# Optimization experiments

Measured on AMD Instinct MI355X. Metric: run time of the kernel, lower is better.

## Reference

```python
import jax, jax.numpy as jnp
from jax import lax
import numpy as np

B, L = 4096, 512
H = 32       # GRU hidden_dim
HH = 32      # hazard_hidden_dim
EPS = 1e-8


def setup_inputs() -> dict:
    key = jax.random.key(0)
    ks = jax.random.split(key, 12)
    s_ih = 1.0 / np.sqrt(H)
    s_l1 = 1.0 / np.sqrt(1 + H)
    s_l2 = 1.0 / np.sqrt(HH)
    return {
        "deltas": jax.random.uniform(ks[0], (B, L), dtype=jnp.float32),
        "mask": jnp.ones((B, L), dtype=jnp.float32),
        # GRUCell params (torch layout: [3H, in], [3H, H], biases [3H]; gates r,z,n)
        "w_ih": jax.random.uniform(ks[1], (3 * H, 1), jnp.float32, -s_ih, s_ih),
        "w_hh": jax.random.uniform(ks[2], (3 * H, H), jnp.float32, -s_ih, s_ih),
        "b_ih": jax.random.uniform(ks[3], (3 * H,), jnp.float32, -s_ih, s_ih),
        "b_hh": jax.random.uniform(ks[4], (3 * H,), jnp.float32, -s_ih, s_ih),
        # hazard MLP: Linear(1+H -> HH), tanh, Linear(HH -> 1)
        "w1": jax.random.uniform(ks[5], (HH, 1 + H), jnp.float32, -s_l1, s_l1),
        "b1": jax.random.uniform(ks[6], (HH,), jnp.float32, -s_l1, s_l1),
        "w2": jax.random.uniform(ks[7], (HH,), jnp.float32, -s_l2, s_l2),
        "b2": jax.random.uniform(ks[8], (1,), jnp.float32, -s_l2, s_l2),
    }


def reference(deltas, mask, w_ih, w_hh, b_ih, b_hh, w1, b1, w2, b2):
    dtype = deltas.dtype
    h0 = jnp.zeros((deltas.shape[0], H), dtype)  # init_hidden_scale == 0 -> zeros
    w1_tau = w1[:, 0]      # [HH] weight on tau column
    w1_h = w1[:, 1:]       # [HH, H]

    def step(carry, xs):
        h, tot = carry
        tau, m = xs                                   # each [B]
        # cumulative hazard phi(tau, h) = softplus(MLP([tau; h]))
        pre = tau[:, None] * w1_tau + h @ w1_h.T + b1  # [B, HH]
        a = jnp.tanh(pre)
        raw = a @ w2 + b2[0]                           # [B]
        phi = jax.nn.softplus(raw)
        # analytic d phi / d tau  (== torch.autograd.grad of phi.sum() wrt tau)
        dphi = jax.nn.sigmoid(raw) * (((1.0 - a * a) * w1_tau) @ w2)
        lam = jax.nn.softplus(dphi) + EPS
        tot = tot + jnp.sum((jnp.log(lam) - phi) * m)
        # GRUCell update with input tau (scalar input_size=1)
        gi = tau[:, None] * w_ih[:, 0] + b_ih          # [B, 3H]
        gh = h @ w_hh.T + b_hh                         # [B, 3H]
        i_r, i_z, i_n = jnp.split(gi, 3, axis=1)
        h_r, h_z, h_n = jnp.split(gh, 3, axis=1)
        r = jax.nn.sigmoid(i_r + h_r)
        z = jax.nn.sigmoid(i_z + h_z)
        n = jnp.tanh(i_n + r * h_n)
        new_h = (1.0 - z) * n + z * h
        me = m[:, None]
        h = me * new_h + (1.0 - me) * h
        return (h, tot), None

    (_, tot), _ = lax.scan(step, (h0, jnp.asarray(0.0, dtype)), (deltas.T, mask.T))
    return tot / (jnp.sum(mask) + EPS)
```

## Files before the change

kernel.cpp:

```cpp
#include <hip/hip_runtime.h>
#include <math.h>


constexpr int Bn = 4096;
constexpr int Ln = 512;
constexpr float EPSf = 1e-8f;
constexpr float LOG2E  = 1.44269504088896f;
constexpr float S2     = 2.0f * LOG2E;

typedef _Float16 f16x8 __attribute__((ext_vector_type(8)));
typedef float    f32x4 __attribute__((ext_vector_type(4)));

__device__ __forceinline__ float aexp2(float x) {
    float r;
    asm volatile("v_exp_f32 %0, %1" : "=v"(r) : "v"(x));
    return r;
}
__device__ __forceinline__ float arcp(float x) {
    float r;
    asm volatile("v_rcp_f32 %0, %1" : "=v"(r) : "v"(x));
    return r;
}

__device__ __forceinline__ float softplusf_(float x) {
    return fmaxf(x, 0.0f) + __logf(1.0f + __expf(-fabsf(x)));
}
__device__ __forceinline__ float sigmoidf_(float x) {
    return __fdividef(1.0f, 1.0f + __expf(-x));
}

union PK2 { _Float16 f[2]; unsigned u; };

__global__ __launch_bounds__(128, 1)
void tpp_main(const float* __restrict__ deltas,
              const float* __restrict__ mask,
              const float* __restrict__ w_ih,
              const float* __restrict__ w_hh,
              const float* __restrict__ b_ih,
              const float* __restrict__ b_hh,
              const float* __restrict__ w1,
              const float* __restrict__ b1,
              const float* __restrict__ w2,
              const float* __restrict__ b2,
              float* __restrict__ partials)
{
    const int tid = threadIdx.x;
    const int w   = tid >> 6;
    const int l   = tid & 63;
    const int c   = l & 15;
    const int g   = l >> 4;
    const int b0  = blockIdx.x * 16;

    __shared__ float2   tm[16][514];
    __shared__ unsigned ibuf[16 * 520];
    __shared__ f16x8    bfbuf[2][16][16][5];

    for (int q = tid; q < 16 * 128; q += 128) {
        const int cc = q >> 7;
        const int t4 = (q & 127) << 2;
        const float4 dv = *(const float4*)(deltas + (size_t)(b0 + cc) * Ln + t4);
        const float4 mv = *(const float4*)(mask   + (size_t)(b0 + cc) * Ln + t4);
        tm[cc][t4 + 0] = make_float2(dv.x, mv.x);
        tm[cc][t4 + 1] = make_float2(dv.y, mv.y);
        tm[cc][t4 + 2] = make_float2(dv.z, mv.z);
        tm[cc][t4 + 3] = make_float2(dv.w, mv.w);
    }

    f16x8 Af[6];
    float wrAn[8], wrBn[8], wzAn[8], wzBn[8];
    float wnA[8], wnB[8];
    f32x4 Cn0 = {}, Cn1 = {};
    float hreg[8];
    f16x8 Afp[2];
    float wpA[8], wpB[8];
    float w2v[8], civ[8], civs = 0.0f, b2v = 0.0f;

    const int ub = 8 * (c >> 2) + (c & 3);
    const int j0 = 8 * g;
    if (w == 0) {
#pragma unroll
        for (int T = 0; T < 6; ++T) {
            const int G = T >> 1, p = T & 1;
            const int up = ub + 4 * p;
            const float sc = (G < 2) ? -LOG2E : S2;
            const float* src =
                (G == 0) ? (w_hh + (size_t)up * 32 + j0) :
                (G == 1) ? (w_hh + (size_t)(32 + up) * 32 + j0) :
                           (w_hh + (size_t)(64 + up) * 32 + j0);
#pragma unroll
            for (int e = 0; e < 8; ++e) Af[T][e] = (_Float16)(src[e] * sc);
        }
#pragma unroll
        for (int e = 0; e < 8; ++e) {
            const int u = 8 * g + e;
            wrAn[e] = -w_ih[u] * LOG2E;
            wrBn[e] = -(b_ih[u] + b_hh[u]) * LOG2E;
            wzAn[e] = -w_ih[32 + u] * LOG2E;
            wzBn[e] = -(b_ih[32 + u] + b_hh[32 + u]) * LOG2E;
            wnA[e]  = w_ih[64 + u] * S2;
            wnB[e]  = b_ih[64 + u] * S2;
            hreg[e] = 0.0f;
        }
#pragma unroll
        for (int d = 0; d < 4; ++d) {
            Cn0[d] = b_hh[64 + 8 * g + d] * S2;
            Cn1[d] = b_hh[64 + 8 * g + 4 + d] * S2;
        }
    } else {
#pragma unroll
        for (int p = 0; p < 2; ++p) {
            const int up = ub + 4 * p;
            const float* src = w1 + (size_t)up * 33 + 1 + j0;
#pragma unroll
            for (int e = 0; e < 8; ++e) Afp[p][e] = (_Float16)(src[e] * S2);
        }
#pragma unroll
        for (int e = 0; e < 8; ++e) {
            const int u = 8 * g + e;
            wpA[e] = w1[(size_t)u * 33] * S2;
            wpB[e] = b1[u] * S2;
            w2v[e] = w2[u];
            civ[e] = w1[(size_t)u * 33] * w2v[e];
            civs  += civ[e];
        }
        b2v = b2[0];
    }

    __syncthreads();

    constexpr int NC = Ln / 16;

    f32x4 Cr0, Cr1, Cz0, Cz1;
    float nbase[8];
    float mcur = 0.0f;
    if (w == 0) {
        const float2 t0v = tm[c][0];
        mcur = t0v.y;
#pragma unroll
        for (int d = 0; d < 4; ++d) {
            Cr0[d] = fmaf(t0v.x, wrAn[d],     wrBn[d]);
            Cr1[d] = fmaf(t0v.x, wrAn[4 + d], wrBn[4 + d]);
            Cz0[d] = fmaf(t0v.x, wzAn[d],     wzBn[d]);
            Cz1[d] = fmaf(t0v.x, wzAn[4 + d], wzBn[4 + d]);
        }
#pragma unroll
        for (int e = 0; e < 8; ++e) nbase[e] = fmaf(t0v.x, wnA[e], wnB[e]);
    }

    for (int chunk = 0; chunk <= NC; ++chunk) {
        if (w == 0 && chunk < NC) {
            const int tbase = chunk * 16;
            for (int s = 0; s < 16; ++s) {
                const int t = tbase + s;

                f16x8 bf;
#pragma unroll
                for (int e2 = 0; e2 < 4; ++e2) {
                    const auto pp = __builtin_amdgcn_cvt_pkrtz(hreg[2 * e2], hreg[2 * e2 + 1]);
                    bf[2 * e2]     = (_Float16)pp[0];
                    bf[2 * e2 + 1] = (_Float16)pp[1];
                }
                bfbuf[chunk & 1][s][c][g] = bf;

                f32x4 ar0 = __builtin_amdgcn_mfma_f32_16x16x32_f16(Af[0], bf, Cr0, 0, 0, 0);
                f32x4 ar1 = __builtin_amdgcn_mfma_f32_16x16x32_f16(Af[1], bf, Cr1, 0, 0, 0);
                f32x4 az0 = __builtin_amdgcn_mfma_f32_16x16x32_f16(Af[2], bf, Cz0, 0, 0, 0);
                f32x4 az1 = __builtin_amdgcn_mfma_f32_16x16x32_f16(Af[3], bf, Cz1, 0, 0, 0);
                f32x4 an0 = __builtin_amdgcn_mfma_f32_16x16x32_f16(Af[4], bf, Cn0, 0, 0, 0);
                f32x4 an1 = __builtin_amdgcn_mfma_f32_16x16x32_f16(Af[5], bf, Cn1, 0, 0, 0);

                const float2 tmn = tm[c][(t + 1 < Ln) ? (t + 1) : t];
                f32x4 Nr0, Nr1, Nz0, Nz1;
                float nbn[8];
#pragma unroll
                for (int d = 0; d < 4; ++d) {
                    Nr0[d] = fmaf(tmn.x, wrAn[d],     wrBn[d]);
                    Nr1[d] = fmaf(tmn.x, wrAn[4 + d], wrBn[4 + d]);
                    Nz0[d] = fmaf(tmn.x, wzAn[d],     wzBn[d]);
                    Nz1[d] = fmaf(tmn.x, wzAn[4 + d], wzBn[4 + d]);
                }
#pragma unroll
                for (int e = 0; e < 8; ++e) nbn[e] = fmaf(tmn.x, wnA[e], wnB[e]);

                float er[8], ez[8];
#pragma unroll
                for (int d = 0; d < 4; ++d) er[d]     = aexp2(ar0[d]);
#pragma unroll
                for (int d = 0; d < 4; ++d) er[4 + d] = aexp2(ar1[d]);
#pragma unroll
                for (int d = 0; d < 4; ++d) ez[d]     = aexp2(az0[d]);
#pragma unroll
                for (int d = 0; d < 4; ++d) ez[4 + d] = aexp2(az1[d]);

                float ar_[8], az_[8], inv[8];
#pragma unroll
                for (int e = 0; e < 8; ++e) { ar_[e] = 1.0f + er[e]; az_[e] = 1.0f + ez[e]; }
#pragma unroll
                for (int e = 0; e < 8; ++e) inv[e] = arcp(ar_[e] * az_[e]);
                float rg[8], zg[8];
#pragma unroll
                for (int e = 0; e < 8; ++e) { rg[e] = inv[e] * az_[e]; zg[e] = inv[e] * ar_[e]; }

                float npe[8];
#pragma unroll
                for (int e = 0; e < 8; ++e) {
                    const float accn = (e < 4) ? an0[e] : an1[e - 4];
                    npe[e] = fmaf(rg[e], accn, nbase[e]);
                }
                float nex[8];
#pragma unroll
                for (int e = 0; e < 8; ++e) nex[e] = aexp2(npe[e]);
                float nrc[8];
#pragma unroll
                for (int e = 0; e < 8; ++e) nrc[e] = arcp(1.0f + nex[e]);

#pragma unroll
                for (int e = 0; e < 8; ++e) {
                    const float nn = fmaf(-2.0f, nrc[e], 1.0f);
                    const float q  = fmaf(-zg[e], mcur, mcur);
                    hreg[e] = fmaf(q, nn - hreg[e], hreg[e]);
                }

                Cr0 = Nr0; Cr1 = Nr1; Cz0 = Nz0; Cz1 = Nz1;
#pragma unroll
                for (int e = 0; e < 8; ++e) nbase[e] = nbn[e];
                mcur = tmn.y;
            }
        } else if (w == 1 && chunk > 0) {
            const int tbase = (chunk - 1) * 16;
            const int rb    = (chunk - 1) & 1;
#pragma unroll 2
            for (int s = 0; s < 16; ++s) {
                const f16x8 bfv = bfbuf[rb][s][c][g];
                const float tau = tm[c][tbase + s].x;
                f32x4 Cp0, Cp1;
#pragma unroll
                for (int d = 0; d < 4; ++d) {
                    Cp0[d] = fmaf(tau, wpA[d],     wpB[d]);
                    Cp1[d] = fmaf(tau, wpA[4 + d], wpB[4 + d]);
                }
                const f32x4 a0 = __builtin_amdgcn_mfma_f32_16x16x32_f16(Afp[0], bfv, Cp0, 0, 0, 0);
                const f32x4 a1 = __builtin_amdgcn_mfma_f32_16x16x32_f16(Afp[1], bfv, Cp1, 0, 0, 0);
                float aex[8];
#pragma unroll
                for (int e = 0; e < 8; ++e) aex[e] = aexp2((e < 4) ? a0[e] : a1[e - 4]);
                float arc[8];
#pragma unroll
                for (int e = 0; e < 8; ++e) arc[e] = arcp(1.0f + aex[e]);
                float v1p = 0.0f, v2p = civs;
#pragma unroll
                for (int e = 0; e < 8; ++e) {
                    const float a = fmaf(-2.0f, arc[e], 1.0f);
                    v1p = fmaf(a, w2v[e], v1p);
                    v2p = fmaf(a * a, -civ[e], v2p);
                }
                v1p += __shfl_xor(v1p, 16, 64);
                v1p += __shfl_xor(v1p, 32, 64);
                v2p += __shfl_xor(v2p, 16, 64);
                v2p += __shfl_xor(v2p, 32, 64);
                if (l < 16) {
                    PK2 pk;
                    pk.f[0] = (_Float16)(v1p + b2v);
                    pk.f[1] = (_Float16)v2p;
                    ibuf[l * 520 + tbase + s] = pk.u;
                }
            }
        }
        __syncthreads();
    }

    float T = 0.0f, M = 0.0f;
#pragma unroll 4
    for (int it = 0; it < 64; ++it) {
        const int idx = it * 128 + tid;
        const int cc  = idx >> 9;
        const int tt  = idx & 511;
        PK2 pk; pk.u = ibuf[cc * 520 + tt];
        const float raw = (float)pk.f[0];
        const float v2  = (float)pk.f[1];
        const float mm  = tm[cc][tt].y;
        const float phi  = softplusf_(raw);
        const float dphi = sigmoidf_(raw) * v2;
        const float lam  = softplusf_(dphi) + EPSf;
        T = fmaf(__logf(lam) - phi, mm, T);
        M += mm;
    }
#pragma unroll
    for (int d = 1; d < 64; d <<= 1) {
        T += __shfl_xor(T, d, 64);
        M += __shfl_xor(M, d, 64);
    }
    __shared__ float sT[2], sM[2];
    if (l == 0) { sT[w] = T; sM[w] = M; }
    __syncthreads();
    if (tid == 0) {
        partials[blockIdx.x]             = sT[0] + sT[1];
        partials[gridDim.x + blockIdx.x] = sM[0] + sM[1];
    }
}

__global__ __launch_bounds__(256)
void tpp_final(const float* __restrict__ partials, int nparts,
               float* __restrict__ out)
{
    const int tid = threadIdx.x;
    double T = 0.0, M = 0.0;
    for (int k = tid; k < nparts; k += 256) {
        T += (double)partials[k];
        M += (double)partials[nparts + k];
    }
#pragma unroll
    for (int d = 1; d < 64; d <<= 1) {
        T += __shfl_xor(T, d, 64);
        M += __shfl_xor(M, d, 64);
    }
    __shared__ double sT[4], sM[4];
    const int w = tid >> 6;
    if ((tid & 63) == 0) { sT[w] = T; sM[w] = M; }
    __syncthreads();
    if (tid == 0) {
        const double t2 = sT[0] + sT[1] + sT[2] + sT[3];
        const double m2 = sM[0] + sM[1] + sM[2] + sM[3];
        out[0] = (float)(t2 / (m2 + (double)EPSf));
    }
}

extern "C" void kernel_launch(void* const* d_in, const int* in_sizes, int n_in,
                              void* d_out, int out_size, void* d_ws, size_t ws_size,
                              hipStream_t stream) {
    const float* deltas = (const float*)d_in[0];
    const float* mask   = (const float*)d_in[1];
    const float* w_ih   = (const float*)d_in[2];
    const float* w_hh   = (const float*)d_in[3];
    const float* b_ih   = (const float*)d_in[4];
    const float* b_hh   = (const float*)d_in[5];
    const float* w1     = (const float*)d_in[6];
    const float* b1     = (const float*)d_in[7];
    const float* w2     = (const float*)d_in[8];
    const float* b2     = (const float*)d_in[9];
    float* out = (float*)d_out;
    float* partials = (float*)d_ws;

    const int nblocks = Bn / 16;
    tpp_main<<<nblocks, 128, 0, stream>>>(deltas, mask, w_ih, w_hh, b_ih, b_hh,
                                          w1, b1, w2, b2, partials);
    tpp_final<<<1, 256, 0, stream>>>(partials, nblocks, out);
}
```

Measured before the change: 252.8 us.

## Split GRU step across two waves with per-step LDS exchange and barriers

Moves from a two-wave design (GRU wave, hazard wave, chunked) to three waves. One wave runs the MFMAs and the z-gate math, a second wave does the r-gate and n-gate transcendentals, and a third runs the hazard MLP 16 steps behind. The two GRU waves swap accumulators and n values through LDS with two block barriers per timestep. Reciprocals are also batched in pairs to save rcp instructions. The aim is to shorten the serial per-step critical path by running exp/rcp work in parallel, at the cost of 1024+ block-wide syncs and LDS round-trips on the recurrence path.

```diff
diff --git a/kernel.cpp b/kernel.cpp
--- a/kernel.cpp
+++ b/kernel.cpp
@@ -21,6 +21,19 @@
     asm volatile("v_rcp_f32 %0, %1" : "=v"(r) : "v"(x));
     return r;
 }
+__device__ __forceinline__ void rcp8_pair(const float* ex, float* out) {
+    float a[8];
+#pragma unroll
+    for (int e = 0; e < 8; ++e) a[e] = 1.0f + ex[e];
+    float inv[4];
+#pragma unroll
+    for (int p = 0; p < 4; ++p) inv[p] = arcp(a[2 * p] * a[2 * p + 1]);
+#pragma unroll
+    for (int p = 0; p < 4; ++p) {
+        out[2 * p]     = inv[p] * a[2 * p + 1];
+        out[2 * p + 1] = inv[p] * a[2 * p];
+    }
+}
 
 __device__ __forceinline__ float softplusf_(float x) {
     return fmaxf(x, 0.0f) + __logf(1.0f + __expf(-fabsf(x)));
@@ -31,7 +44,7 @@
 
 union PK2 { _Float16 f[2]; unsigned u; };
 
-__global__ __launch_bounds__(128, 1)
+__global__ __launch_bounds__(192, 1)
 void tpp_main(const float* __restrict__ deltas,
               const float* __restrict__ mask,
               const float* __restrict__ w_ih,
@@ -53,9 +66,11 @@
 
     __shared__ float2   tm[16][514];
     __shared__ unsigned ibuf[16 * 520];
-    __shared__ f16x8    bfbuf[2][16][16][5];
-
-    for (int q = tid; q < 16 * 128; q += 128) {
+    __shared__ f16x8    bfring[2][16][16][5];
+    __shared__ __align__(16) float accb[64][20];
+    __shared__ __align__(16) float nnb[64][12];
+
+    for (int q = tid; q < 16 * 128; q += 192) {
         const int cc = q >> 7;
         const int t4 = (q & 127) << 2;
         const float4 dv = *(const float4*)(deltas + (size_t)(b0 + cc) * Ln + t4);
@@ -68,16 +83,16 @@
 
     f16x8 Af[6];
     float wrAn[8], wrBn[8], wzAn[8], wzBn[8];
-    float wnA[8], wnB[8];
     f32x4 Cn0 = {}, Cn1 = {};
     float hreg[8];
+    float wnA[8], wnB[8];
     f16x8 Afp[2];
     float wpA[8], wpB[8];
     float w2v[8], civ[8], civs = 0.0f, b2v = 0.0f;
 
     const int ub = 8 * (c >> 2) + (c & 3);
     const int j0 = 8 * g;
-    if (w == 0) {
+    if (w == 1) {
 #pragma unroll
         for (int T = 0; T < 6; ++T) {
             const int G = T >> 1, p = T & 1;
@@ -97,14 +112,19 @@
             wrBn[e] = -(b_ih[u] + b_hh[u]) * LOG2E;
             wzAn[e] = -w_ih[32 + u] * LOG2E;
             wzBn[e] = -(b_ih[32 + u] + b_hh[32 + u]) * LOG2E;
-            wnA[e]  = w_ih[64 + u] * S2;
-            wnB[e]  = b_ih[64 + u] * S2;
             hreg[e] = 0.0f;
         }
 #pragma unroll
         for (int d = 0; d < 4; ++d) {
             Cn0[d] = b_hh[64 + 8 * g + d] * S2;
             Cn1[d] = b_hh[64 + 8 * g + 4 + d] * S2;
+        }
+    } else if (w == 0) {
+#pragma unroll
+        for (int e = 0; e < 8; ++e) {
+            const int u = 8 * g + e;
+            wnA[e] = w_ih[64 + u] * S2;
+            wnB[e] = b_ih[64 + u] * S2;
         }
     } else {
 #pragma unroll
@@ -128,12 +148,9 @@
 
     __syncthreads();
 
-    constexpr int NC = Ln / 16;
-
     f32x4 Cr0, Cr1, Cz0, Cz1;
-    float nbase[8];
     float mcur = 0.0f;
-    if (w == 0) {
+    if (w == 1) {
         const float2 t0v = tm[c][0];
         mcur = t0v.y;
 #pragma unroll
@@ -143,138 +160,138 @@
             Cz0[d] = fmaf(t0v.x, wzAn[d],     wzBn[d]);
             Cz1[d] = fmaf(t0v.x, wzAn[4 + d], wzBn[4 + d]);
         }
-#pragma unroll
-        for (int e = 0; e < 8; ++e) nbase[e] = fmaf(t0v.x, wnA[e], wnB[e]);
-    }
-
-    for (int chunk = 0; chunk <= NC; ++chunk) {
-        if (w == 0 && chunk < NC) {
-            const int tbase = chunk * 16;
-            for (int s = 0; s < 16; ++s) {
-                const int t = tbase + s;
-
-                f16x8 bf;
-#pragma unroll
-                for (int e2 = 0; e2 < 4; ++e2) {
-                    const auto pp = __builtin_amdgcn_cvt_pkrtz(hreg[2 * e2], hreg[2 * e2 + 1]);
-                    bf[2 * e2]     = (_Float16)pp[0];
-                    bf[2 * e2 + 1] = (_Float16)pp[1];
-                }
-                bfbuf[chunk & 1][s][c][g] = bf;
-
-                f32x4 ar0 = __builtin_amdgcn_mfma_f32_16x16x32_f16(Af[0], bf, Cr0, 0, 0, 0);
-                f32x4 ar1 = __builtin_amdgcn_mfma_f32_16x16x32_f16(Af[1], bf, Cr1, 0, 0, 0);
-                f32x4 az0 = __builtin_amdgcn_mfma_f32_16x16x32_f16(Af[2], bf, Cz0, 0, 0, 0);
-                f32x4 az1 = __builtin_amdgcn_mfma_f32_16x16x32_f16(Af[3], bf, Cz1, 0, 0, 0);
-                f32x4 an0 = __builtin_amdgcn_mfma_f32_16x16x32_f16(Af[4], bf, Cn0, 0, 0, 0);
-                f32x4 an1 = __builtin_amdgcn_mfma_f32_16x16x32_f16(Af[5], bf, Cn1, 0, 0, 0);
-
-                const float2 tmn = tm[c][(t + 1 < Ln) ? (t + 1) : t];
-                f32x4 Nr0, Nr1, Nz0, Nz1;
-                float nbn[8];
-#pragma unroll
-                for (int d = 0; d < 4; ++d) {
-                    Nr0[d] = fmaf(tmn.x, wrAn[d],     wrBn[d]);
-                    Nr1[d] = fmaf(tmn.x, wrAn[4 + d], wrBn[4 + d]);
-                    Nz0[d] = fmaf(tmn.x, wzAn[d],     wzBn[d]);
-                    Nz1[d] = fmaf(tmn.x, wzAn[4 + d], wzBn[4 + d]);
-                }
-#pragma unroll
-                for (int e = 0; e < 8; ++e) nbn[e] = fmaf(tmn.x, wnA[e], wnB[e]);
-
-                float er[8], ez[8];
-#pragma unroll
-                for (int d = 0; d < 4; ++d) er[d]     = aexp2(ar0[d]);
-#pragma unroll
-                for (int d = 0; d < 4; ++d) er[4 + d] = aexp2(ar1[d]);
-#pragma unroll
-                for (int d = 0; d < 4; ++d) ez[d]     = aexp2(az0[d]);
-#pragma unroll
-                for (int d = 0; d < 4; ++d) ez[4 + d] = aexp2(az1[d]);
-
-                float ar_[8], az_[8], inv[8];
-#pragma unroll
-                for (int e = 0; e < 8; ++e) { ar_[e] = 1.0f + er[e]; az_[e] = 1.0f + ez[e]; }
-#pragma unroll
-                for (int e = 0; e < 8; ++e) inv[e] = arcp(ar_[e] * az_[e]);
-                float rg[8], zg[8];
-#pragma unroll
-                for (int e = 0; e < 8; ++e) { rg[e] = inv[e] * az_[e]; zg[e] = inv[e] * ar_[e]; }
-
-                float npe[8];
-#pragma unroll
-                for (int e = 0; e < 8; ++e) {
-                    const float accn = (e < 4) ? an0[e] : an1[e - 4];
-                    npe[e] = fmaf(rg[e], accn, nbase[e]);
-                }
-                float nex[8];
-#pragma unroll
-                for (int e = 0; e < 8; ++e) nex[e] = aexp2(npe[e]);
-                float nrc[8];
-#pragma unroll
-                for (int e = 0; e < 8; ++e) nrc[e] = arcp(1.0f + nex[e]);
-
-#pragma unroll
-                for (int e = 0; e < 8; ++e) {
-                    const float nn = fmaf(-2.0f, nrc[e], 1.0f);
-                    const float q  = fmaf(-zg[e], mcur, mcur);
-                    hreg[e] = fmaf(q, nn - hreg[e], hreg[e]);
-                }
-
-                Cr0 = Nr0; Cr1 = Nr1; Cz0 = Nz0; Cz1 = Nz1;
-#pragma unroll
-                for (int e = 0; e < 8; ++e) nbase[e] = nbn[e];
-                mcur = tmn.y;
-            }
-        } else if (w == 1 && chunk > 0) {
-            const int tbase = (chunk - 1) * 16;
-            const int rb    = (chunk - 1) & 1;
-#pragma unroll 2
-            for (int s = 0; s < 16; ++s) {
-                const f16x8 bfv = bfbuf[rb][s][c][g];
-                const float tau = tm[c][tbase + s].x;
-                f32x4 Cp0, Cp1;
-#pragma unroll
-                for (int d = 0; d < 4; ++d) {
-                    Cp0[d] = fmaf(tau, wpA[d],     wpB[d]);
-                    Cp1[d] = fmaf(tau, wpA[4 + d], wpB[4 + d]);
-                }
-                const f32x4 a0 = __builtin_amdgcn_mfma_f32_16x16x32_f16(Afp[0], bfv, Cp0, 0, 0, 0);
-                const f32x4 a1 = __builtin_amdgcn_mfma_f32_16x16x32_f16(Afp[1], bfv, Cp1, 0, 0, 0);
-                float aex[8];
-#pragma unroll
-                for (int e = 0; e < 8; ++e) aex[e] = aexp2((e < 4) ? a0[e] : a1[e - 4]);
-                float arc[8];
-#pragma unroll
-                for (int e = 0; e < 8; ++e) arc[e] = arcp(1.0f + aex[e]);
-                float v1p = 0.0f, v2p = civs;
-#pragma unroll
-                for (int e = 0; e < 8; ++e) {
-                    const float a = fmaf(-2.0f, arc[e], 1.0f);
-                    v1p = fmaf(a, w2v[e], v1p);
-                    v2p = fmaf(a * a, -civ[e], v2p);
-                }
-                v1p += __shfl_xor(v1p, 16, 64);
-                v1p += __shfl_xor(v1p, 32, 64);
-                v2p += __shfl_xor(v2p, 16, 64);
-                v2p += __shfl_xor(v2p, 32, 64);
-                if (l < 16) {
-                    PK2 pk;
-                    pk.f[0] = (_Float16)(v1p + b2v);
-                    pk.f[1] = (_Float16)v2p;
-                    ibuf[l * 520 + tbase + s] = pk.u;
-                }
-            }
+    }
+
+    f32x4 az0, az1;
+    float qm[8];
+
+    for (int t = 0; t < Ln + 16; ++t) {
+        if (w == 1 && t < Ln) {
+            f16x8 bf;
+#pragma unroll
+            for (int e2 = 0; e2 < 4; ++e2) {
+                const auto pp = __builtin_amdgcn_cvt_pkrtz(hreg[2 * e2], hreg[2 * e2 + 1]);
+                bf[2 * e2]     = (_Float16)pp[0];
+                bf[2 * e2 + 1] = (_Float16)pp[1];
+            }
+            bfring[(t >> 4) & 1][t & 15][c][g] = bf;
+            const f32x4 ar0 = __builtin_amdgcn_mfma_f32_16x16x32_f16(Af[0], bf, Cr0, 0, 0, 0);
+            const f32x4 ar1 = __builtin_amdgcn_mfma_f32_16x16x32_f16(Af[1], bf, Cr1, 0, 0, 0);
+            az0 = __builtin_amdgcn_mfma_f32_16x16x32_f16(Af[2], bf, Cz0, 0, 0, 0);
+            az1 = __builtin_amdgcn_mfma_f32_16x16x32_f16(Af[3], bf, Cz1, 0, 0, 0);
+            const f32x4 an0 = __builtin_amdgcn_mfma_f32_16x16x32_f16(Af[4], bf, Cn0, 0, 0, 0);
+            const f32x4 an1 = __builtin_amdgcn_mfma_f32_16x16x32_f16(Af[5], bf, Cn1, 0, 0, 0);
+            *(f32x4*)&accb[l][0]  = ar0;
+            *(f32x4*)&accb[l][4]  = ar1;
+            *(f32x4*)&accb[l][8]  = an0;
+            *(f32x4*)&accb[l][12] = an1;
         }
         __syncthreads();
+
+        if (w == 0 && t < Ln) {
+            const float tau = tm[c][t].x;
+            float nbase[8];
+#pragma unroll
+            for (int e = 0; e < 8; ++e) nbase[e] = fmaf(tau, wnA[e], wnB[e]);
+            const f32x4 ar0 = *(const f32x4*)&accb[l][0];
+            const f32x4 ar1 = *(const f32x4*)&accb[l][4];
+            const f32x4 an0 = *(const f32x4*)&accb[l][8];
+            const f32x4 an1 = *(const f32x4*)&accb[l][12];
+            float er[8];
+#pragma unroll
+            for (int d = 0; d < 4; ++d) er[d]     = aexp2(ar0[d]);
+#pragma unroll
+            for (int d = 0; d < 4; ++d) er[4 + d] = aexp2(ar1[d]);
+            float rg[8];
+            rcp8_pair(er, rg);
+            float nex[8];
+#pragma unroll
+            for (int e = 0; e < 8; ++e) {
+                const float accn = (e < 4) ? an0[e] : an1[e - 4];
+                nex[e] = aexp2(fmaf(rg[e], accn, nbase[e]));
+            }
+            float nrc[8];
+            rcp8_pair(nex, nrc);
+            f32x4 nn0, nn1;
+#pragma unroll
+            for (int d = 0; d < 4; ++d) {
+                nn0[d] = fmaf(-2.0f, nrc[d],     1.0f);
+                nn1[d] = fmaf(-2.0f, nrc[4 + d], 1.0f);
+            }
+            *(f32x4*)&nnb[l][0] = nn0;
+            *(f32x4*)&nnb[l][4] = nn1;
+        } else if (w == 1 && t < Ln) {
+            float ez[8];
+#pragma unroll
+            for (int d = 0; d < 4; ++d) ez[d]     = aexp2(az0[d]);
+#pragma unroll
+            for (int d = 0; d < 4; ++d) ez[4 + d] = aexp2(az1[d]);
+            float zg[8];
+            rcp8_pair(ez, zg);
+#pragma unroll
+            for (int e = 0; e < 8; ++e) qm[e] = fmaf(-zg[e], mcur, mcur);
+            const int tn = (t + 1 < Ln) ? (t + 1) : t;
+            const float2 tmn = tm[c][tn];
+#pragma unroll
+            for (int d = 0; d < 4; ++d) {
+                Cr0[d] = fmaf(tmn.x, wrAn[d],     wrBn[d]);
+                Cr1[d] = fmaf(tmn.x, wrAn[4 + d], wrBn[4 + d]);
+                Cz0[d] = fmaf(tmn.x, wzAn[d],     wzBn[d]);
+                Cz1[d] = fmaf(tmn.x, wzAn[4 + d], wzBn[4 + d]);
+            }
+            mcur = tmn.y;
+        } else if (w == 2 && t >= 16) {
+            const int tp = t - 16;
+            const f16x8 bfv = bfring[(tp >> 4) & 1][tp & 15][c][g];
+            const float tau = tm[c][tp].x;
+            f32x4 Cp0, Cp1;
+#pragma unroll
+            for (int d = 0; d < 4; ++d) {
+                Cp0[d] = fmaf(tau, wpA[d],     wpB[d]);
+                Cp1[d] = fmaf(tau, wpA[4 + d], wpB[4 + d]);
+            }
+            const f32x4 a0 = __builtin_amdgcn_mfma_f32_16x16x32_f16(Afp[0], bfv, Cp0, 0, 0, 0);
+            const f32x4 a1 = __builtin_amdgcn_mfma_f32_16x16x32_f16(Afp[1], bfv, Cp1, 0, 0, 0);
+            float aex[8];
+#pragma unroll
+            for (int e = 0; e < 8; ++e) aex[e] = aexp2((e < 4) ? a0[e] : a1[e - 4]);
+            float arc[8];
+            rcp8_pair(aex, arc);
+            float v1p = 0.0f, v2p = civs;
+#pragma unroll
+            for (int e = 0; e < 8; ++e) {
+                const float a = fmaf(-2.0f, arc[e], 1.0f);
+                v1p = fmaf(a, w2v[e], v1p);
+                v2p = fmaf(a * a, -civ[e], v2p);
+            }
+            v1p += __shfl_xor(v1p, 16, 64);
+            v1p += __shfl_xor(v1p, 32, 64);
+            v2p += __shfl_xor(v2p, 16, 64);
+            v2p += __shfl_xor(v2p, 32, 64);
+            if (l < 16) {
+                PK2 pk;
+                pk.f[0] = (_Float16)(v1p + b2v);
+                pk.f[1] = (_Float16)v2p;
+                ibuf[l * 520 + tp] = pk.u;
+            }
+        }
+        __syncthreads();
+
+        if (w == 1 && t < Ln) {
+            const f32x4 nn0 = *(const f32x4*)&nnb[l][0];
+            const f32x4 nn1 = *(const f32x4*)&nnb[l][4];
+#pragma unroll
+            for (int e = 0; e < 8; ++e) {
+                const float nn = (e < 4) ? nn0[e] : nn1[e - 4];
+                hreg[e] = fmaf(qm[e], nn - hreg[e], hreg[e]);
+            }
+        }
     }
 
     float T = 0.0f, M = 0.0f;
-#pragma unroll 4
-    for (int it = 0; it < 64; ++it) {
-        const int idx = it * 128 + tid;
-        const int cc  = idx >> 9;
-        const int tt  = idx & 511;
+    for (int idx = tid; idx < 16 * 512; idx += 192) {
+        const int cc = idx >> 9;
+        const int tt = idx & 511;
         PK2 pk; pk.u = ibuf[cc * 520 + tt];
         const float raw = (float)pk.f[0];
         const float v2  = (float)pk.f[1];
@@ -290,12 +307,12 @@
         T += __shfl_xor(T, d, 64);
         M += __shfl_xor(M, d, 64);
     }
-    __shared__ float sT[2], sM[2];
+    __shared__ float sT[3], sM[3];
     if (l == 0) { sT[w] = T; sM[w] = M; }
     __syncthreads();
     if (tid == 0) {
-        partials[blockIdx.x]             = sT[0] + sT[1];
-        partials[gridDim.x + blockIdx.x] = sM[0] + sM[1];
+        partials[blockIdx.x]             = sT[0] + sT[1] + sT[2];
+        partials[gridDim.x + blockIdx.x] = sM[0] + sM[1] + sM[2];
     }
 }
 
@@ -342,7 +359,7 @@
     float* partials = (float*)d_ws;
 
     const int nblocks = Bn / 16;
-    tpp_main<<<nblocks, 128, 0, stream>>>(deltas, mask, w_ih, w_hh, b_ih, b_hh,
+    tpp_main<<<nblocks, 192, 0, stream>>>(deltas, mask, w_ih, w_hh, b_ih, b_hh,
                                           w1, b1, w2, b2, partials);
     tpp_final<<<1, 256, 0, stream>>>(partials, nblocks, out);
 }
```

Measured after the change: 353.1 us. 1.4x slower.
